# Performance work log

Measured on AMD Instinct MI355X. Metric: run time of the kernel, lower is better.

Reference implementation:

```python
import jax, jax.numpy as jnp
import numpy as np

LN2 = jnp.log(jnp.float32(2.0))
ALPHA = 0.5          # alpha_pool = [0.5]
A_BITS = 8           # activation bit width (BIT_TYPE_A)
W_BITS = 8           # weight bit width (BIT_TYPE_W)
EPS = 1e-8


def round_ln(x):
    # 'round' branch: floor(log2(x)) then pick nearer power of two
    y = jnp.floor(jnp.log(x) / LN2)
    up = (x - 2.0 ** y) > (2.0 ** (y + 1.0) - x)
    return y + up.astype(x.dtype)


def fq_act_asym(x, bits=A_BITS):
    # per-tensor asymmetric uniform fake-quant (QAct min-max observer)
    qmax = 2 ** bits - 1
    xmin = jnp.minimum(x.min(), 0.0)
    xmax = jnp.maximum(x.max(), 0.0)
    scale = jnp.maximum((xmax - xmin) / qmax, EPS)
    zp = jnp.round(-xmin / scale)
    q = jnp.clip(jnp.round(x / scale) + zp, 0, qmax)
    return (q - zp) * scale


def fq_act_sym(x, bits=A_BITS):
    # per-tensor symmetric fake-quant (qact1 with asymmetric=False)
    qmax = 2 ** (bits - 1) - 1
    scale = jnp.maximum(jnp.abs(x).max() / qmax, EPS)
    q = jnp.clip(jnp.round(x / scale), -qmax - 1, qmax)
    return q * scale


def fq_weight(w, bits=W_BITS):
    # per-output-channel symmetric weight fake-quant (QLinear)
    qmax = 2 ** (bits - 1) - 1
    scale = jnp.maximum(jnp.abs(w).max(axis=1, keepdims=True) / qmax, EPS)
    q = jnp.clip(jnp.round(w / scale), -qmax - 1, qmax)
    return q * scale


def setup_inputs() -> dict:
    key = jax.random.key(0)
    ks = jax.random.split(key, 5)
    B, N, C, H = 64, 197, 768, 3072
    x = jax.random.normal(ks[0], (B, N, C), dtype=jnp.float32)
    w1 = jax.random.normal(ks[1], (H, C), dtype=jnp.float32) * 0.02
    b1 = jax.random.normal(ks[2], (H,), dtype=jnp.float32) * 0.02
    w2 = jax.random.normal(ks[3], (C, H), dtype=jnp.float32) * 0.02
    b2 = jax.random.normal(ks[4], (C,), dtype=jnp.float32) * 0.02
    return {"x": x, "w1": w1, "b1": b1, "w2": w2, "b2": b2}


def reference(x, w1, b1, w2, b2):
    # ---- smoothquant power-of-two channel scale (fc1 input channels) ----
    global_max_x = jnp.abs(x).max(axis=(0, 1))      # [C]
    max_weight = jnp.abs(w1).max(axis=0)            # [C]
    cs = global_max_x ** ALPHA / max_weight ** (1.0 - ALPHA)
    cs = 2.0 ** round_ln(cs)                        # snap to power of two
    x_smoothed = x / cs[None, None, :]
    w1_smoothed = w1 * cs[None, :]
    # ---- qact0 -> fc1 (8-bit fake-quant GEMM) ----
    xq = fq_act_asym(x_smoothed)
    h = jnp.einsum('bnc,hc->bnh', xq, fq_weight(w1_smoothed)) + b1
    # ---- act (exact GELU, nn.GELU default) -> qact1 (symmetric) ----
    h = jax.nn.gelu(h, approximate=False)
    hq = fq_act_sym(h)
    # ---- fc2 -> qact2 ----
    out = jnp.einsum('bnh,ch->bnc', hq, fq_weight(w2)) + b2
    out = fq_act_asym(out)
    return out
```

## Files before the change

kernel.cpp:

```cpp
#include <hip/hip_runtime.h>
#include <cstdint>
#include <cstddef>

typedef int v4i __attribute__((ext_vector_type(4)));

#define DI static __device__ __forceinline__

DI unsigned fmap(float f){ unsigned b=__float_as_uint(f); return (b&0x80000000u)? ~b : (b|0x80000000u); }
DI float funmap(unsigned u){ return (u&0x80000000u)? __uint_as_float(u&0x7fffffffu) : __uint_as_float(~u); }
DI float gelu_f(float x){ return 0.5f*x*(1.0f+erff(x*0.70710678118654752440f)); }

constexpr int Mtok = 12608;
constexpr int Cdim = 768;
constexpr int Hdim = 3072;
constexpr int MP   = 12672;

__global__ void k_init(unsigned* scal, unsigned* xminU, unsigned* xmaxU, unsigned* wmaxU){
    int t = blockIdx.x*256 + threadIdx.x;
    if (t < Cdim){
        xminU[t] = fmap(__builtin_inff());
        xmaxU[t] = fmap(-__builtin_inff());
        wmaxU[t] = fmap(0.0f);
    }
    if (t == 0){
        scal[0] = fmap(0.0f);
        scal[1] = fmap(__builtin_inff());
        scal[2] = fmap(-__builtin_inff());
    }
}

__global__ void k_colstats_x(const float* __restrict__ x, unsigned* xminU, unsigned* xmaxU){
    int t = threadIdx.x;
    float mn0= __builtin_inff(), mn1= __builtin_inff(), mn2= __builtin_inff();
    float mx0=-__builtin_inff(), mx1=-__builtin_inff(), mx2=-__builtin_inff();
    for (int r = blockIdx.x; r < Mtok; r += gridDim.x){
        const float* row = x + (size_t)r*Cdim;
        float v0=row[t], v1=row[t+256], v2=row[t+512];
        mn0=fminf(mn0,v0); mx0=fmaxf(mx0,v0);
        mn1=fminf(mn1,v1); mx1=fmaxf(mx1,v1);
        mn2=fminf(mn2,v2); mx2=fmaxf(mx2,v2);
    }
    atomicMin(&xminU[t      ], fmap(mn0)); atomicMax(&xmaxU[t      ], fmap(mx0));
    atomicMin(&xminU[t+256  ], fmap(mn1)); atomicMax(&xmaxU[t+256  ], fmap(mx1));
    atomicMin(&xminU[t+512  ], fmap(mn2)); atomicMax(&xmaxU[t+512  ], fmap(mx2));
}

__global__ void k_colmax_w1(const float* __restrict__ w1, unsigned* wmaxU){
    int t = threadIdx.x;
    float m0=0.f, m1=0.f, m2=0.f;
    for (int r = blockIdx.x; r < Hdim; r += gridDim.x){
        const float* row = w1 + (size_t)r*Cdim;
        m0=fmaxf(m0,fabsf(row[t]));
        m1=fmaxf(m1,fabsf(row[t+256]));
        m2=fmaxf(m2,fabsf(row[t+512]));
    }
    atomicMax(&wmaxU[t      ], fmap(m0));
    atomicMax(&wmaxU[t+256  ], fmap(m1));
    atomicMax(&wmaxU[t+512  ], fmap(m2));
}

__global__ void k_scale0(const unsigned* xminU, const unsigned* xmaxU, const unsigned* wmaxU,
                         float* cs, unsigned* scal){
    __shared__ float smn[256], smx[256];
    int t = threadIdx.x;
    float lmn =  __builtin_inff(), lmx = -__builtin_inff();
    #pragma unroll
    for (int j = 0; j < 3; ++j){
        int c = t + j*256;
        float xn = funmap(xminU[c]), xm = funmap(xmaxU[c]), wm = funmap(wmaxU[c]);
        float g  = fmaxf(fabsf(xn), fabsf(xm));
        float csr = powf(g, 0.5f) / powf(wm, 0.5f);
        float y = floorf(logf(csr) / 0.6931471805599453f);
        float p = exp2f(y);
        float c2 = exp2f(y + (((csr - p) > (2.0f*p - csr)) ? 1.0f : 0.0f));
        cs[c] = c2;
        lmn = fminf(lmn, xn / c2);
        lmx = fmaxf(lmx, xm / c2);
    }
    smn[t]=lmn; smx[t]=lmx; __syncthreads();
    for (int s=128; s; s>>=1){
        if (t < s){ smn[t]=fminf(smn[t],smn[t+s]); smx[t]=fmaxf(smx[t],smx[t+s]); }
        __syncthreads();
    }
    if (t == 0){
        float xmin_t = fminf(smn[0], 0.0f);
        float xmax_t = fmaxf(smx[0], 0.0f);
        float sc = fmaxf((xmax_t - xmin_t)/255.0f, 1e-8f);
        float zp = rintf(-xmin_t/sc);
        float* fs = (float*)scal;
        fs[8] = sc; fs[9] = zp;
    }
}

__global__ void k_quant_w1(const float* __restrict__ w1, const float* __restrict__ cs,
                           const unsigned* scal, int8_t* __restrict__ qw1,
                           float* sa1, int* icorr1){
    __shared__ float sm[256];
    __shared__ int   si[256];
    int h = blockIdx.x, t = threadIdx.x;
    const float* wr = w1 + (size_t)h*Cdim;
    float v0 = wr[t]*cs[t], v1 = wr[t+256]*cs[t+256], v2 = wr[t+512]*cs[t+512];
    float am = fmaxf(fabsf(v0), fmaxf(fabsf(v1), fabsf(v2)));
    sm[t]=am; __syncthreads();
    for (int s=128; s; s>>=1){ if (t<s) sm[t]=fmaxf(sm[t],sm[t+s]); __syncthreads(); }
    float scale = fmaxf(sm[0]/127.0f, 1e-8f);
    float q0 = fminf(fmaxf(rintf(v0/scale), -128.0f), 127.0f);
    float q1 = fminf(fmaxf(rintf(v1/scale), -128.0f), 127.0f);
    float q2 = fminf(fmaxf(rintf(v2/scale), -128.0f), 127.0f);
    qw1[(size_t)h*Cdim + t      ] = (int8_t)q0;
    qw1[(size_t)h*Cdim + t + 256] = (int8_t)q1;
    qw1[(size_t)h*Cdim + t + 512] = (int8_t)q2;
    si[t] = (int)q0 + (int)q1 + (int)q2; __syncthreads();
    for (int s=128; s; s>>=1){ if (t<s) si[t]+=si[t+s]; __syncthreads(); }
    if (t == 0){
        const float* fs = (const float*)scal;
        sa1[h]    = fs[8]*scale;
        icorr1[h] = (128 - (int)fs[9]) * si[0];
    }
}

__global__ void k_quant_w2(const float* __restrict__ w2, int8_t* __restrict__ qw2, float* sa2){
    __shared__ float sm[256];
    int c = blockIdx.x, t = threadIdx.x;
    const float* wr = w2 + (size_t)c*Hdim;
    float v[12]; float am = 0.f;
    #pragma unroll
    for (int j=0;j<12;++j){ v[j]=wr[t + j*256]; am=fmaxf(am,fabsf(v[j])); }
    sm[t]=am; __syncthreads();
    for (int s=128; s; s>>=1){ if (t<s) sm[t]=fmaxf(sm[t],sm[t+s]); __syncthreads(); }
    float scale = fmaxf(sm[0]/127.0f, 1e-8f);
    #pragma unroll
    for (int j=0;j<12;++j){
        float q = fminf(fmaxf(rintf(v[j]/scale), -128.0f), 127.0f);
        qw2[(size_t)c*Hdim + t + j*256] = (int8_t)q;
    }
    if (t == 0) sa2[c] = scale;
}

__global__ void k_quant_x(const float* __restrict__ x, const float* __restrict__ cs,
                          const unsigned* scal, int8_t* __restrict__ qxs){
    int idx = blockIdx.x*256 + threadIdx.x;
    const int total = Mtok*(Cdim/4);
    if (idx >= total) return;
    const float* fs = (const float*)scal;
    float sc = fs[8], zp = fs[9];
    float4 v = ((const float4*)x)[idx];
    int cb = (idx % (Cdim/4))*4;
    float q0 = fminf(fmaxf(rintf((v.x/cs[cb+0])/sc)+zp, 0.f), 255.f);
    float q1 = fminf(fmaxf(rintf((v.y/cs[cb+1])/sc)+zp, 0.f), 255.f);
    float q2 = fminf(fmaxf(rintf((v.z/cs[cb+2])/sc)+zp, 0.f), 255.f);
    float q3 = fminf(fmaxf(rintf((v.w/cs[cb+3])/sc)+zp, 0.f), 255.f);
    uint32_t pack =  (uint32_t)(uint8_t)((int)q0-128)
                  | ((uint32_t)(uint8_t)((int)q1-128) << 8)
                  | ((uint32_t)(uint8_t)((int)q2-128) << 16)
                  | ((uint32_t)(uint8_t)((int)q3-128) << 24);
    ((uint32_t*)qxs)[idx] = pack;
}

#define GLL(src,dst) __builtin_amdgcn_global_load_lds( \
    (const __attribute__((address_space(1))) unsigned*)(src), \
    (__attribute__((address_space(3))) unsigned*)(dst), 16, 0, 0)

template<int KSTEPS, int MODE>
__global__ __launch_bounds__(256)
void k_gemm(const int8_t* __restrict__ A, const int8_t* __restrict__ Bw, int N,
            const float* __restrict__ sa, const int* __restrict__ icorr,
            const float* __restrict__ bias, const unsigned* __restrict__ scal,
            int8_t* __restrict__ qout, float* __restrict__ fout,
            unsigned* __restrict__ r0, unsigned* __restrict__ r1)
{
    constexpr int K = KSTEPS*64;
    __shared__ __align__(16) int8_t As[8192];
    __shared__ __align__(16) int8_t Bs[8192];
    __shared__ float sred[8];
    int t = threadIdx.x, lane = t & 63, wid = t >> 6;
    int wr = wid >> 1, wc = wid & 1;
    size_t brow = (size_t)blockIdx.x * 128;
    int bcol = blockIdx.y * 128;

    int srow = t >> 2;
    int schunk = (t & 3) ^ ((srow >> 1) & 3);
    const int8_t* ga0 = A  + (brow + srow)*(size_t)K + schunk*16;
    const int8_t* gb0 = Bw + (size_t)(bcol + srow)*K + schunk*16;

    int rsw  = ((lane >> 4) ^ ((lane >> 1) & 3)) << 4;
    int aoff = ((wr*64 + (lane & 15)) << 6) + rsw;
    int boff = ((wc*64 + (lane & 15)) << 6) + rsw;

    v4i acc[4][4] = {};
    for (int ks = 0; ks < KSTEPS; ++ks){
        __syncthreads();
        const int8_t* pa = ga0 + ks*64;
        const int8_t* pb = gb0 + ks*64;
        GLL(pa,                   As + t*16);
        GLL(pa + (size_t)64*K,    As + 4096 + t*16);
        GLL(pb,                   Bs + t*16);
        GLL(pb + (size_t)64*K,    Bs + 4096 + t*16);
        __syncthreads();
        v4i a[4], b[4];
        #pragma unroll
        for (int m=0;m<4;++m) a[m] = *(const v4i*)(As + aoff + (m<<10));
        #pragma unroll
        for (int n=0;n<4;++n) b[n] = *(const v4i*)(Bs + boff + (n<<10));
        #pragma unroll
        for (int m=0;m<4;++m)
            #pragma unroll
            for (int n=0;n<4;++n)
                acc[m][n] = __builtin_amdgcn_mfma_i32_16x16x64_i8(a[m], b[n], acc[m][n], 0, 0, 0);
    }

    int rl = (lane >> 4) * 4;
    if (MODE == 0){
        float amax = 0.f;
        #pragma unroll
        for (int n=0;n<4;++n){
            int col = bcol + wc*64 + n*16 + (lane & 15);
            float s = sa[col]; int ic = icorr[col]; float bb = bias[col];
            #pragma unroll
            for (int m=0;m<4;++m){
                size_t row = brow + wr*64 + m*16 + rl;
                #pragma unroll
                for (int r=0;r<4;++r){
                    if (row + r < (size_t)Mtok){
                        float g = gelu_f(s*(float)(acc[m][n][r] + ic) + bb);
                        amax = fmaxf(amax, fabsf(g));
                    }
                }
            }
        }
        #pragma unroll
        for (int off=32; off; off>>=1) amax = fmaxf(amax, __shfl_down(amax, off));
        if (lane == 0) sred[wid] = amax;
        __syncthreads();
        if (t == 0) atomicMax(r0, fmap(fmaxf(fmaxf(sred[0],sred[1]), fmaxf(sred[2],sred[3]))));
    } else if (MODE == 1){
        float sh = fmaxf(funmap(*scal)/127.0f, 1e-8f);
        #pragma unroll
        for (int n=0;n<4;++n){
            int col = bcol + wc*64 + n*16 + (lane & 15);
            float s = sa[col]; int ic = icorr[col]; float bb = bias[col];
            #pragma unroll
            for (int m=0;m<4;++m){
                size_t row = brow + wr*64 + m*16 + rl;
                #pragma unroll
                for (int r=0;r<4;++r){
                    if (row + r < (size_t)Mtok){
                        float g = gelu_f(s*(float)(acc[m][n][r] + ic) + bb);
                        float q = fminf(fmaxf(rintf(g/sh), -128.0f), 127.0f);
                        qout[(row + r)*(size_t)N + col] = (int8_t)q;
                    }
                }
            }
        }
    } else {
        float sh = fmaxf(funmap(*scal)/127.0f, 1e-8f);
        float lmin =  __builtin_inff(), lmax = -__builtin_inff();
        #pragma unroll
        for (int n=0;n<4;++n){
            int col = bcol + wc*64 + n*16 + (lane & 15);
            float s = sh * sa[col]; float bb = bias[col];
            #pragma unroll
            for (int m=0;m<4;++m){
                size_t row = brow + wr*64 + m*16 + rl;
                #pragma unroll
                for (int r=0;r<4;++r){
                    if (row + r < (size_t)Mtok){
                        float o = s*(float)acc[m][n][r] + bb;
                        fout[(row + r)*(size_t)N + col] = o;
                        lmin = fminf(lmin, o); lmax = fmaxf(lmax, o);
                    }
                }
            }
        }
        #pragma unroll
        for (int off=32; off; off>>=1){
            lmin = fminf(lmin, __shfl_down(lmin, off));
            lmax = fmaxf(lmax, __shfl_down(lmax, off));
        }
        if (lane == 0){ sred[wid] = lmin; sred[4+wid] = lmax; }
        __syncthreads();
        if (t == 0){
            atomicMin(r0, fmap(fminf(fminf(sred[0],sred[1]), fminf(sred[2],sred[3]))));
            atomicMax(r1, fmap(fmaxf(fmaxf(sred[4],sred[5]), fmaxf(sred[6],sred[7]))));
        }
    }
}

__global__ void k_final(const float* __restrict__ outpre, const unsigned* __restrict__ scal,
                        float* __restrict__ out){
    int idx = blockIdx.x*256 + threadIdx.x;
    const int total = Mtok*(Cdim/4);
    if (idx >= total) return;
    float omin = fminf(funmap(scal[1]), 0.0f);
    float omax = fmaxf(funmap(scal[2]), 0.0f);
    float sc = fmaxf((omax - omin)/255.0f, 1e-8f);
    float zp = rintf(-omin/sc);
    float4 v = ((const float4*)outpre)[idx];
    v.x = (fminf(fmaxf(rintf(v.x/sc)+zp, 0.f), 255.f) - zp)*sc;
    v.y = (fminf(fmaxf(rintf(v.y/sc)+zp, 0.f), 255.f) - zp)*sc;
    v.z = (fminf(fmaxf(rintf(v.z/sc)+zp, 0.f), 255.f) - zp)*sc;
    v.w = (fminf(fmaxf(rintf(v.w/sc)+zp, 0.f), 255.f) - zp)*sc;
    ((float4*)out)[idx] = v;
}

extern "C" void kernel_launch(void* const* d_in, const int* in_sizes, int n_in,
                              void* d_out, int out_size, void* d_ws, size_t ws_size,
                              hipStream_t stream)
{
    if (n_in < 5) return;
    const float* x  = (const float*)d_in[0];
    const float* w1 = (const float*)d_in[1];
    const float* b1 = (const float*)d_in[2];
    const float* w2 = (const float*)d_in[3];
    const float* b2 = (const float*)d_in[4];
    float* out = (float*)d_out;

    uint8_t* w = (uint8_t*)d_ws;
    size_t off = 0;
    unsigned* scal  = (unsigned*)(w + off); off += 256;
    unsigned* xminU = (unsigned*)(w + off); off += 3072;
    unsigned* xmaxU = (unsigned*)(w + off); off += 3072;
    unsigned* wmaxU = (unsigned*)(w + off); off += 3072;
    float*    cs    = (float*)   (w + off); off += 3072;
    float*    sa1   = (float*)   (w + off); off += 12288;
    int*      icorr1= (int*)     (w + off); off += 12288;
    float*    sa2   = (float*)   (w + off); off += 3072;
    off = (off + 255) & ~(size_t)255;
    int8_t*   qw1   = (int8_t*)  (w + off); off += (size_t)Hdim*Cdim;
    int8_t*   qw2   = (int8_t*)  (w + off); off += (size_t)Cdim*Hdim;
    int8_t*   qxs   = (int8_t*)  (w + off); off += (size_t)MP*Cdim;
    int8_t*   qh    = (int8_t*)  (w + off); off += (size_t)MP*Hdim;
    float*    outpre= (float*)   (w + off); off += (size_t)Mtok*Cdim*4;
    if (ws_size < off) return;

    k_init<<<3, 256, 0, stream>>>(scal, xminU, xmaxU, wmaxU);
    k_colstats_x<<<512, 256, 0, stream>>>(x, xminU, xmaxU);
    k_colmax_w1<<<512, 256, 0, stream>>>(w1, wmaxU);
    k_scale0<<<1, 256, 0, stream>>>(xminU, xmaxU, wmaxU, cs, scal);
    k_quant_w1<<<Hdim, 256, 0, stream>>>(w1, cs, scal, qw1, sa1, icorr1);
    k_quant_w2<<<Cdim, 256, 0, stream>>>(w2, qw2, sa2);
    k_quant_x<<<(Mtok*(Cdim/4) + 255)/256, 256, 0, stream>>>(x, cs, scal, qxs);

    k_gemm<12,0><<<dim3(99,24), 256, 0, stream>>>(qxs, qw1, Hdim, sa1, icorr1, b1, scal,
                                                  nullptr, nullptr, &scal[0], nullptr);
    k_gemm<12,1><<<dim3(99,24), 256, 0, stream>>>(qxs, qw1, Hdim, sa1, icorr1, b1, scal,
                                                  qh, nullptr, nullptr, nullptr);
    k_gemm<48,2><<<dim3(99,6), 256, 0, stream>>>(qh, qw2, Cdim, sa2, nullptr, b2, scal,
                                                 nullptr, outpre, &scal[1], &scal[2]);

    k_final<<<(Mtok*(Cdim/4) + 255)/256, 256, 0, stream>>>(outpre, scal, out);
}
```

Measured before the change: 424.0 us.

## Double-buffer GEMM LDS, swizzle blocks across XCDs, cache fp16 GELU instead of recomputing fc1

The GEMM main loop now uses two LDS buffers so global-to-LDS loads for the next k-step overlap the MFMA work on the current one. A 1D grid is remapped so that consecutive tiles land on the same XCD, which should improve L2 reuse. When the workspace is large enough, the second fc1 GEMM pass is replaced by one pass that writes fp16 GELU output and reduces amax, followed by an elementwise requantize kernel. This trades a full recompute of fc1 for roughly 77MB of extra fp16 traffic, and quantizing from fp16 instead of fp32 can shift some int8 rounding results.

```diff
diff --git a/kernel.cpp b/kernel.cpp
--- a/kernel.cpp
+++ b/kernel.cpp
@@ -161,22 +161,30 @@
     (const __attribute__((address_space(1))) unsigned*)(src), \
     (__attribute__((address_space(3))) unsigned*)(dst), 16, 0, 0)
 
-template<int KSTEPS, int MODE>
+template<int KSTEPS, int MODE, int NY>
 __global__ __launch_bounds__(256)
 void k_gemm(const int8_t* __restrict__ A, const int8_t* __restrict__ Bw, int N,
             const float* __restrict__ sa, const int* __restrict__ icorr,
             const float* __restrict__ bias, const unsigned* __restrict__ scal,
-            int8_t* __restrict__ qout, float* __restrict__ fout,
+            int8_t* __restrict__ qout, float* __restrict__ fout, _Float16* __restrict__ hout,
             unsigned* __restrict__ r0, unsigned* __restrict__ r1)
 {
     constexpr int K = KSTEPS*64;
-    __shared__ __align__(16) int8_t As[8192];
-    __shared__ __align__(16) int8_t Bs[8192];
+    __shared__ __align__(16) int8_t As0[8192];
+    __shared__ __align__(16) int8_t Bs0[8192];
+    __shared__ __align__(16) int8_t As1[8192];
+    __shared__ __align__(16) int8_t Bs1[8192];
     __shared__ float sred[8];
     int t = threadIdx.x, lane = t & 63, wid = t >> 6;
     int wr = wid >> 1, wc = wid & 1;
-    size_t brow = (size_t)blockIdx.x * 128;
-    int bcol = blockIdx.y * 128;
+
+    int nwg = gridDim.x;
+    int q8 = nwg >> 3, r8 = nwg & 7;
+    int xcd = blockIdx.x & 7, li = blockIdx.x >> 3;
+    int swz = (xcd < r8 ? xcd*(q8+1) : r8*(q8+1) + (xcd - r8)*q8) + li;
+    int bx = swz / NY, by = swz % NY;
+    size_t brow = (size_t)bx * 128;
+    int bcol = by * 128;
 
     int srow = t >> 2;
     int schunk = (t & 3) ^ ((srow >> 1) & 3);
@@ -188,25 +196,38 @@
     int boff = ((wc*64 + (lane & 15)) << 6) + rsw;
 
     v4i acc[4][4] = {};
-    for (int ks = 0; ks < KSTEPS; ++ks){
-        __syncthreads();
-        const int8_t* pa = ga0 + ks*64;
-        const int8_t* pb = gb0 + ks*64;
-        GLL(pa,                   As + t*16);
-        GLL(pa + (size_t)64*K,    As + 4096 + t*16);
-        GLL(pb,                   Bs + t*16);
-        GLL(pb + (size_t)64*K,    Bs + 4096 + t*16);
-        __syncthreads();
-        v4i a[4], b[4];
-        #pragma unroll
-        for (int m=0;m<4;++m) a[m] = *(const v4i*)(As + aoff + (m<<10));
-        #pragma unroll
-        for (int n=0;n<4;++n) b[n] = *(const v4i*)(Bs + boff + (n<<10));
-        #pragma unroll
-        for (int m=0;m<4;++m)
-            #pragma unroll
-            for (int n=0;n<4;++n)
-                acc[m][n] = __builtin_amdgcn_mfma_i32_16x16x64_i8(a[m], b[n], acc[m][n], 0, 0, 0);
+
+#define STAGE(AS,BS,ks) do{ \
+    const int8_t* pa_ = ga0 + (ks)*64; \
+    const int8_t* pb_ = gb0 + (ks)*64; \
+    GLL(pa_,                   AS + t*16); \
+    GLL(pa_ + (size_t)64*K,    AS + 4096 + t*16); \
+    GLL(pb_,                   BS + t*16); \
+    GLL(pb_ + (size_t)64*K,    BS + 4096 + t*16); \
+}while(0)
+
+#define COMPUTE(AS,BS) do{ \
+    v4i a_[4], b_[4]; \
+    _Pragma("unroll") \
+    for (int m=0;m<4;++m) a_[m] = *(const v4i*)(AS + aoff + (m<<10)); \
+    _Pragma("unroll") \
+    for (int n=0;n<4;++n) b_[n] = *(const v4i*)(BS + boff + (n<<10)); \
+    _Pragma("unroll") \
+    for (int m=0;m<4;++m) \
+        _Pragma("unroll") \
+        for (int n=0;n<4;++n) \
+            acc[m][n] = __builtin_amdgcn_mfma_i32_16x16x64_i8(a_[m], b_[n], acc[m][n], 0, 0, 0); \
+}while(0)
+
+    STAGE(As0,Bs0,0);
+    __syncthreads();
+    for (int ks = 0; ks < KSTEPS; ks += 2){
+        STAGE(As1,Bs1,ks+1);
+        COMPUTE(As0,Bs0);
+        __syncthreads();
+        if (ks + 2 < KSTEPS) STAGE(As0,Bs0,ks+2);
+        COMPUTE(As1,Bs1);
+        __syncthreads();
     }
 
     int rl = (lane >> 4) * 4;
@@ -246,12 +267,36 @@
                 for (int r=0;r<4;++r){
                     if (row + r < (size_t)Mtok){
                         float g = gelu_f(s*(float)(acc[m][n][r] + ic) + bb);
-                        float q = fminf(fmaxf(rintf(g/sh), -128.0f), 127.0f);
-                        qout[(row + r)*(size_t)N + col] = (int8_t)q;
+                        float qv = fminf(fmaxf(rintf(g/sh), -128.0f), 127.0f);
+                        qout[(row + r)*(size_t)N + col] = (int8_t)qv;
                     }
                 }
             }
         }
+    } else if (MODE == 3){
+        float amax = 0.f;
+        #pragma unroll
+        for (int n=0;n<4;++n){
+            int col = bcol + wc*64 + n*16 + (lane & 15);
+            float s = sa[col]; int ic = icorr[col]; float bb = bias[col];
+            #pragma unroll
+            for (int m=0;m<4;++m){
+                size_t row = brow + wr*64 + m*16 + rl;
+                #pragma unroll
+                for (int r=0;r<4;++r){
+                    if (row + r < (size_t)Mtok){
+                        float g = gelu_f(s*(float)(acc[m][n][r] + ic) + bb);
+                        amax = fmaxf(amax, fabsf(g));
+                        hout[(row + r)*(size_t)N + col] = (_Float16)g;
+                    }
+                }
+            }
+        }
+        #pragma unroll
+        for (int off=32; off; off>>=1) amax = fmaxf(amax, __shfl_down(amax, off));
+        if (lane == 0) sred[wid] = amax;
+        __syncthreads();
+        if (t == 0) atomicMax(r0, fmap(fmaxf(fmaxf(sred[0],sred[1]), fmaxf(sred[2],sred[3]))));
     } else {
         float sh = fmaxf(funmap(*scal)/127.0f, 1e-8f);
         float lmin =  __builtin_inff(), lmax = -__builtin_inff();
@@ -284,6 +329,31 @@
             atomicMax(r1, fmap(fmaxf(fmaxf(sred[4],sred[5]), fmaxf(sred[6],sred[7]))));
         }
     }
+#undef STAGE
+#undef COMPUTE
+}
+
+struct alignas(16) H8 { _Float16 v[8]; };
+__global__ void k_requant(const _Float16* __restrict__ h, const unsigned* __restrict__ scal,
+                          int8_t* __restrict__ qh){
+    int idx = blockIdx.x*256 + threadIdx.x;
+    const int total = Mtok*(Hdim/8);
+    if (idx >= total) return;
+    float sh = fmaxf(funmap(scal[0])/127.0f, 1e-8f);
+    H8 h8 = ((const H8*)h)[idx];
+    uint32_t lo = 0, hi = 0;
+    #pragma unroll
+    for (int j=0;j<4;++j){
+        float qv = fminf(fmaxf(rintf((float)h8.v[j]/sh), -128.0f), 127.0f);
+        lo |= ((uint32_t)(uint8_t)(int)qv) << (8*j);
+    }
+    #pragma unroll
+    for (int j=0;j<4;++j){
+        float qv = fminf(fmaxf(rintf((float)h8.v[4+j]/sh), -128.0f), 127.0f);
+        hi |= ((uint32_t)(uint8_t)(int)qv) << (8*j);
+    }
+    uint2 pk; pk.x = lo; pk.y = hi;
+    ((uint2*)qh)[idx] = pk;
 }
 
 __global__ void k_final(const float* __restrict__ outpre, const unsigned* __restrict__ scal,
@@ -330,8 +400,13 @@
     int8_t*   qw2   = (int8_t*)  (w + off); off += (size_t)Cdim*Hdim;
     int8_t*   qxs   = (int8_t*)  (w + off); off += (size_t)MP*Cdim;
     int8_t*   qh    = (int8_t*)  (w + off); off += (size_t)MP*Hdim;
-    float*    outpre= (float*)   (w + off); off += (size_t)Mtok*Cdim*4;
-    if (ws_size < off) return;
+    size_t off_big = off;
+    float*    outpre= (float*)   (w + off_big);
+    _Float16* hbuf  = (_Float16*)(w + off_big);
+    size_t need_3g  = off_big + (size_t)Mtok*Cdim*4;
+    size_t need_h16 = off_big + (size_t)Mtok*Hdim*2;
+    if (ws_size < need_3g) return;
+    bool use_h16 = (ws_size >= need_h16);
 
     k_init<<<3, 256, 0, stream>>>(scal, xminU, xmaxU, wmaxU);
     k_colstats_x<<<512, 256, 0, stream>>>(x, xminU, xmaxU);
@@ -341,12 +416,18 @@
     k_quant_w2<<<Cdim, 256, 0, stream>>>(w2, qw2, sa2);
     k_quant_x<<<(Mtok*(Cdim/4) + 255)/256, 256, 0, stream>>>(x, cs, scal, qxs);
 
-    k_gemm<12,0><<<dim3(99,24), 256, 0, stream>>>(qxs, qw1, Hdim, sa1, icorr1, b1, scal,
-                                                  nullptr, nullptr, &scal[0], nullptr);
-    k_gemm<12,1><<<dim3(99,24), 256, 0, stream>>>(qxs, qw1, Hdim, sa1, icorr1, b1, scal,
-                                                  qh, nullptr, nullptr, nullptr);
-    k_gemm<48,2><<<dim3(99,6), 256, 0, stream>>>(qh, qw2, Cdim, sa2, nullptr, b2, scal,
-                                                 nullptr, outpre, &scal[1], &scal[2]);
+    if (use_h16){
+        k_gemm<12,3,24><<<2376, 256, 0, stream>>>(qxs, qw1, Hdim, sa1, icorr1, b1, scal,
+                                                  nullptr, nullptr, hbuf, &scal[0], nullptr);
+        k_requant<<<(Mtok*(Hdim/8) + 255)/256, 256, 0, stream>>>(hbuf, scal, qh);
+    } else {
+        k_gemm<12,0,24><<<2376, 256, 0, stream>>>(qxs, qw1, Hdim, sa1, icorr1, b1, scal,
+                                                  nullptr, nullptr, nullptr, &scal[0], nullptr);
+        k_gemm<12,1,24><<<2376, 256, 0, stream>>>(qxs, qw1, Hdim, sa1, icorr1, b1, scal,
+                                                  qh, nullptr, nullptr, nullptr, nullptr);
+    }
+    k_gemm<48,2,6><<<594, 256, 0, stream>>>(qh, qw2, Cdim, sa2, nullptr, b2, scal,
+                                            nullptr, outpre, nullptr, &scal[1], &scal[2]);
 
     k_final<<<(Mtok*(Cdim/4) + 255)/256, 256, 0, stream>>>(outpre, scal, out);
 }
```

Result: faster. 382.0 us (-9.9%).
